# Kernel optimization log

Hardware: AMD Instinct MI355X
Metric: run time of the kernel (lower is better)

The kernel has to match this reference:

```python
import jax, jax.numpy as jnp
import numpy as np

EPS = 1e-6

def oneplus(x):
    return 1.0 + jnp.log1p(jnp.exp(x) + EPS)

def content_addr(mem, keys, strength):
    # mem [B,N,M], keys [B,R,M], strength [B,R] -> [B,R,N]
    mn = jnp.sqrt(jnp.sum(mem * mem, -1))    # [B,N]
    kn = jnp.sqrt(jnp.sum(keys * keys, -1))  # [B,R]
    sim = jnp.einsum('brm,bnm->brn', keys, mem) / (kn[..., None] * mn[:, None, :] + EPS)
    return jax.nn.softmax(strength[..., None] * sim, axis=-1)

def setup_inputs() -> dict:
    key = jax.random.key(0)
    ks = jax.random.split(key, 16)
    B, T, W, R, N, M = 16, 32, 128, 4, 512, 128
    def lin(k, fi, fo):
        k1, k2 = jax.random.split(k)
        s = 1.0 / np.sqrt(fi)
        return (jax.random.uniform(k1, (fi, fo), minval=-s, maxval=s),
                jax.random.uniform(k2, (fo,), minval=-s, maxval=s))
    Din = W + R * W  # controller input: cat(x_t, prev_reads)
    Wb, bb = lin(ks[0], Din + W, W)     # CfC backbone (1 layer, silu)
    Wff1, bff1 = lin(ks[1], W, W)
    Wff2, bff2 = lin(ks[2], W, W)
    Wta, bta = lin(ks[3], W, W)
    Wtb, btb = lin(ks[4], W, W)
    Wv, bv = lin(ks[5], W, W)
    Wr, br = lin(ks[6], W * R, W)
    Wxi, bxi = lin(ks[7], W, W * R + 3 * W + 5 * R + 3)
    X = jax.random.normal(ks[8], (B, T, W), dtype=jnp.float32)
    hs = jnp.zeros((B, W), dtype=jnp.float32)
    mem = jax.random.normal(ks[9], (B, N, M), dtype=jnp.float32) * 0.1
    reset_idxs = jax.random.randint(ks[10], (B, T), 0, 2, dtype=jnp.int32)
    return {'X': X, 'hs': hs, 'mem': mem, 'reset_idxs': reset_idxs,
            'Wb': Wb, 'bb': bb, 'Wff1': Wff1, 'bff1': bff1, 'Wff2': Wff2, 'bff2': bff2,
            'Wta': Wta, 'bta': bta, 'Wtb': Wtb, 'btb': btb,
            'Wv': Wv, 'bv': bv, 'Wr': Wr, 'br': br, 'Wxi': Wxi, 'bxi': bxi}

def dnc_forward(X, hs, mem, reset_idxs, Wb, bb, Wff1, bff1, Wff2, bff2,
                Wta, bta, Wtb, btb, Wv, bv, Wr, br, Wxi, bxi):
    B, T, W = X.shape
    N, M = mem.shape[1], mem.shape[2]
    R = (bxi.shape[0] - 3 * W - 3) // (W + 5)
    eye = jnp.eye(N, dtype=mem.dtype)

    def step(carry, inp):
        hs, memv, prev_reads, prev_rw, prev_ww, usage, prec, link = carry
        x_t, reset, t = inp
        r = reset.astype(x_t.dtype)
        memv = memv * (1 - r)[:, None, None]   # memory.reset_idx
        hs = hs * (1 - r)[:, None]
        # CfC controller cell
        z = jax.nn.silu(jnp.concatenate([x_t, prev_reads, hs], -1) @ Wb + bb)
        ff1 = z @ Wff1 + bff1
        ff2 = z @ Wff2 + bff2
        ti = jax.nn.sigmoid((z @ Wta + bta) * t + (z @ Wtb + btb))
        hs = ff1 * (1 - ti) + ti * ff2
        # interface vector split
        xi = hs @ Wxi + bxi
        p = 0
        read_keys = xi[:, :W * R].reshape(B, R, W); p = W * R
        write_key = xi[:, p:p + W]; p += W
        write_vec = xi[:, p:p + W]; p += W
        erase = jax.nn.sigmoid(xi[:, p:p + W]); p += W
        free_g = jax.nn.sigmoid(xi[:, p:p + R]); p += R
        read_str = oneplus(xi[:, p:p + R]); p += R
        read_modes = jax.nn.softmax(xi[:, p:p + 3 * R].reshape(B, R, 3), -1); p += 3 * R
        write_str = oneplus(xi[:, p:p + 1]); p += 1
        alloc_g = jax.nn.sigmoid(xi[:, p:p + 1]); p += 1
        write_g = jax.nn.sigmoid(xi[:, p:p + 1])
        # write weights
        wca = content_addr(memv, write_key[:, None, :], write_str)[:, 0]  # [B,N]
        retention = jnp.prod(1 - free_g[:, :, None] * prev_rw, axis=1)
        usage = (usage + prev_ww - usage * prev_ww) * retention
        si = jnp.argsort(usage, -1)
        cp = jnp.cumprod(jnp.take_along_axis(usage, si, -1), -1)
        alloc = (1 - usage) * jnp.take_along_axis(cp, si, -1)  # gather(1, sorted_idx), as in source
        ww = write_g * (alloc_g * alloc + (1 - alloc_g) * wca)  # [B,N]
        wc = ww[:, :, None]
        link = (1 - wc - jnp.swapaxes(wc, 1, 2)) * link + wc * prec[:, None, :]
        link = link * (1 - eye)
        prec = (1 - ww.sum(-1, keepdims=True)) * prec + ww
        memv = memv * (1 - wc * erase[:, None, :]) + wc * write_vec[:, None, :]
        # read
        rca = content_addr(memv, read_keys, read_str)              # [B,R,N]
        fw = jnp.einsum('brn,bnk->brk', prev_rw, link)
        bw = jnp.einsum('brn,bkn->brk', prev_rw, link)
        aux = jnp.stack([bw, rca, fw], 2)                          # [B,R,3,N]
        rw = (aux * read_modes[..., None]).sum(2)
        reads = jnp.einsum('brn,bnm->brm', rw, memv).reshape(B, R * M)
        y = hs @ Wv + bv + reads @ Wr + br
        # prev_reads is detached each step in the source
        carry = (hs, memv, jax.lax.stop_gradient(reads), rw, ww, usage, prec, link)
        return carry, (y, hs)

    dt = X.dtype
    init = (hs, mem,
            jnp.zeros((B, R * W), dt), jnp.zeros((B, R, N), dt), jnp.zeros((B, N), dt),
            jnp.zeros((B, N), dt), jnp.zeros((B, N), dt), jnp.zeros((B, N, N), dt))
    xs = (jnp.swapaxes(X, 0, 1), jnp.swapaxes(reset_idxs, 0, 1), jnp.arange(T, dtype=dt))
    _, (ys, hss) = jax.lax.scan(step, init, xs)
    return jnp.swapaxes(ys, 0, 1), jnp.swapaxes(hss, 0, 1)

def reference(X, hs, mem, reset_idxs, Wb, bb, Wff1, bff1, Wff2, bff2,
              Wta, bta, Wtb, btb, Wv, bv, Wr, br, Wxi, bxi):
    return dnc_forward(X, hs, mem, reset_idxs, Wb, bb, Wff1, bff1, Wff2, bff2,
                       Wta, bta, Wtb, btb, Wv, bv, Wr, br, Wxi, bxi)
```

## Files before the change

kernel.cpp:

```cpp
#include <hip/hip_runtime.h>
#include <math.h>

#define Bq 16
#define Tq 32
#define Wq 128
#define Rq 4
#define Nq 512
#define Mq 128
#define DINq 768
#define XIDq 919
#define BTWq (Bq*Tq*Wq)

#define TSTRIDE 31232
#define TF_FW    0
#define TF_BW    16384
#define TF_RCA   18432
#define TF_RW    20480
#define TF_PR    22528
#define TF_WC    26624
#define TF_WW    27136
#define TF_PREC  27648
#define TF_XI    28672
#define TF_CNT   29696

struct P {
  const float *X, *hs0, *mem0;
  const int *rst;
  const float *Wb,*bb,*Wff1,*bff1,*Wff2,*bff2,*Wta,*bta,*Wtb,*btb,*Wv,*bv,*Wr,*br,*Wxi,*bxi;
  float *out;
  float *rdh,*teams;
  float *WbT,*Wff1T,*Wff2T,*WtaT,*WtbT,*WvT,*WrT,*WxiT;
};

__device__ __forceinline__ float dot4(float4 a, float4 b){
  return a.x*b.x + a.y*b.y + a.z*b.z + a.w*b.w;
}
__device__ __forceinline__ float sigf(float x){ return 1.f/(1.f+expf(-x)); }
__device__ __forceinline__ float oneplusf(float x){ return 1.f + log1pf(expf(x) + 1e-6f); }

__device__ __forceinline__ void pst(float* p, float v){
  __hip_atomic_store(p, v, __ATOMIC_RELAXED, __HIP_MEMORY_SCOPE_AGENT);
}
__device__ __forceinline__ float pld(float* p){
  return __hip_atomic_load(p, __ATOMIC_RELAXED, __HIP_MEMORY_SCOPE_AGENT);
}
__device__ __forceinline__ void bump(unsigned* f){
  __syncthreads();
  if (threadIdx.x==0)
    __hip_atomic_fetch_add(f, 1u, __ATOMIC_RELAXED, __HIP_MEMORY_SCOPE_AGENT);
}
__device__ __forceinline__ void waitge(unsigned* f, unsigned v){
  if (threadIdx.x==0){
    while (__hip_atomic_load(f, __ATOMIC_RELAXED, __HIP_MEMORY_SCOPE_AGENT) < v)
      __builtin_amdgcn_s_sleep(1);
  }
  __syncthreads();
}

__device__ __forceinline__ float wave_sum64(float v){
  #pragma unroll
  for (int m=32;m>=1;m>>=1) v += __shfl_xor(v, m, 64);
  return v;
}
__device__ __forceinline__ float wave_max64(float v){
  #pragma unroll
  for (int m=32;m>=1;m>>=1) v = fmaxf(v, __shfl_xor(v, m, 64));
  return v;
}
__device__ __forceinline__ float blk_sum(float v, float* s8){
  int w = threadIdx.x>>6;
  v = wave_sum64(v);
  if ((threadIdx.x&63)==0) s8[w] = v;
  __syncthreads();
  float r = s8[0]+s8[1]+s8[2]+s8[3]+s8[4]+s8[5]+s8[6]+s8[7];
  __syncthreads();
  return r;
}
__device__ __forceinline__ float blk_max(float v, float* s8){
  int w = threadIdx.x>>6;
  v = wave_max64(v);
  if ((threadIdx.x&63)==0) s8[w] = v;
  __syncthreads();
  float r = s8[0];
  #pragma unroll
  for (int q=1;q<8;q++) r = fmaxf(r, s8[q]);
  __syncthreads();
  return r;
}
__device__ __forceinline__ float red_cg(float v){
  v += __shfl_xor(v, 1, 8);
  v += __shfl_xor(v, 2, 8);
  v += __shfl_xor(v, 4, 8);
  return v;
}

__global__ __launch_bounds__(256) void k_init(P p){
  int bid=blockIdx.x, tid=threadIdx.x;
  if (bid<8){ int idx=bid*256+tid, st=8*256;
    for (int k=idx;k<DINq*Wq;k+=st){ int j=k/DINq,i=k%DINq; p.WbT[k]=p.Wb[i*Wq+j]; }
  } else if (bid<10){ int idx=(bid-8)*256+tid, st=2*256;
    for (int k=idx;k<Wq*Wq;k+=st){ int j=k/Wq,i=k%Wq; p.Wff1T[k]=p.Wff1[i*Wq+j]; }
  } else if (bid<12){ int idx=(bid-10)*256+tid, st=2*256;
    for (int k=idx;k<Wq*Wq;k+=st){ int j=k/Wq,i=k%Wq; p.Wff2T[k]=p.Wff2[i*Wq+j]; }
  } else if (bid<14){ int idx=(bid-12)*256+tid, st=2*256;
    for (int k=idx;k<Wq*Wq;k+=st){ int j=k/Wq,i=k%Wq; p.WtaT[k]=p.Wta[i*Wq+j]; }
  } else if (bid<16){ int idx=(bid-14)*256+tid, st=2*256;
    for (int k=idx;k<Wq*Wq;k+=st){ int j=k/Wq,i=k%Wq; p.WtbT[k]=p.Wtb[i*Wq+j]; }
  } else if (bid<18){ int idx=(bid-16)*256+tid, st=2*256;
    for (int k=idx;k<Wq*Wq;k+=st){ int j=k/Wq,i=k%Wq; p.WvT[k]=p.Wv[i*Wq+j]; }
  } else if (bid<22){ int idx=(bid-18)*256+tid, st=4*256;
    for (int k=idx;k<Rq*Wq*Wq;k+=st){ int j=k/(Rq*Wq),i=k%(Rq*Wq); p.WrT[k]=p.Wr[i*Wq+j]; }
  } else if (bid<30){ int idx=(bid-22)*256+tid, st=8*256;
    for (int k=idx;k<XIDq*Wq;k+=st){ int f=k/Wq,i=k%Wq; p.WxiT[k]=p.Wxi[i*XIDq+f]; }
  } else if (bid<38){ int idx=(bid-30)*256+tid, st=8*256;
    for (int k=idx;k<16*TSTRIDE;k+=st) p.teams[k]=0.f;
  }
}

__global__ __launch_bounds__(512,2) void k_run(P p){
  const int tid=threadIdx.x, bid=blockIdx.x;
  const bool isA = (bid<16);
  const int team = isA ? bid : ((bid-16)>>3);
  const int g    = isA ? 0   : ((bid-16)&7);
  const int b=team;
  const int w=tid>>6, l=tid&63;
  float* T = p.teams + (size_t)team*TSTRIDE;
  unsigned* C = (unsigned*)(T+TF_CNT);
  unsigned* CNT_FW=C+0; unsigned* FLAG_RW=C+32; unsigned* CNT_RD=C+64;
  unsigned* FLAG_XI=C+96; unsigned* CNT_WC=C+128; unsigned* FLAG_WW=C+160;

  __shared__ __align__(16) float rwl[Rq*Nq];
  __shared__ __align__(16) float xil[XIDq+9];
  __shared__ __align__(16) float wwl[Nq];
  __shared__ __align__(16) float precl[Nq];
  __shared__ __align__(16) float usage[Nq];
  __shared__ __align__(16) float uarr[Nq];
  __shared__ __align__(16) float cpl[Nq];
  __shared__ __align__(16) int   sidx[Nq];
  __shared__ __align__(16) float wcas[Nq];
  __shared__ __align__(16) float inv[DINq];
  __shared__ __align__(16) float zl[Wq];
  __shared__ __align__(16) float hsl[Wq];
  __shared__ __align__(16) float acc4[4*Wq];
  __shared__ __align__(16) float scrA[Rq*Nq];
  __shared__ __align__(16) float scrB[Rq*Nq];
  __shared__ __align__(16) float scrC[Rq*Nq];
  __shared__ float s8[8];

  if (isA){
    for (int i=tid;i<Rq*Nq;i+=512) rwl[i]=0.f;
    usage[tid]=0.f; precl[tid]=0.f; wwl[tid]=0.f;
    if (tid<Wq) hsl[tid]=p.hs0[b*Wq+tid];
    __syncthreads();

    for (int t=0;t<=Tq;t++){
      if (t>0){
        waitge(CNT_FW, 8u*(unsigned)t);
        float* rcl=scrA; float* fwl=scrB; float* bwl=scrC;
        #pragma unroll
        for (int k=0;k<4;k++){
          int idx=tid+k*512;
          float f=0.f;
          #pragma unroll
          for (int gg=0;gg<8;gg++) f+=pld(T+TF_FW+gg*2048+idx);
          fwl[idx]=f;
          bwl[idx]=pld(T+TF_BW+idx);
          rcl[idx]=pld(T+TF_RCA+idx);
        }
        __syncthreads();
        #pragma unroll
        for (int r=0;r<Rq;r++){
          float v=rcl[r*Nq+tid];
          float mx=blk_max(v,s8);
          float e=expf(v-mx);
          float se=blk_sum(e,s8);
          rcl[r*Nq+tid]=e/se;
        }
        __syncthreads();
        #pragma unroll
        for (int k=0;k<4;k++){
          int idx=tid+k*512, r=idx>>9;
          float m0=xil[904+r*3],m1=xil[905+r*3],m2=xil[906+r*3];
          float mm=fmaxf(m0,fmaxf(m1,m2));
          float e0=expf(m0-mm),e1=expf(m1-mm),e2=expf(m2-mm);
          float es=e0+e1+e2;
          float rwv=(e0*bwl[idx]+e1*rcl[idx]+e2*fwl[idx])/es;
          rwl[idx]=rwv;
          pst(T+TF_RW+idx,rwv);
        }
      } else {
        #pragma unroll
        for (int k=0;k<4;k++){ int idx=tid+k*512; rwl[idx]=0.f; pst(T+TF_RW+idx,0.f); }
      }
      bump(FLAG_RW);
      if (t<Tq){
        float keep=1.f-(float)p.rst[b*Tq+t];
        if (tid<Wq){ inv[tid]=p.X[((size_t)b*Tq+t)*Wq+tid]; inv[Wq+Nq+tid]=keep*hsl[tid]; }
        __syncthreads();
        int j=tid>>2,q=tid&3;
        const float4* w4=(const float4*)(p.WbT+(size_t)j*DINq);
        const float4* i4=(const float4*)inv;
        float a=0.f;
        #pragma unroll
        for (int c=q;c<32;c+=4) a+=dot4(w4[c],i4[c]);
        #pragma unroll
        for (int c=160+q;c<192;c+=4) a+=dot4(w4[c],i4[c]);
        a+=__shfl_xor(a,1,4); a+=__shfl_xor(a,2,4);
        if (q==0) zl[j]=a+p.bb[j];
      }
      waitge(CNT_RD, 8u*(unsigned)(t+1));
      if (t>0){
        float s=0.f;
        #pragma unroll
        for (int gg=0;gg<8;gg++) s+=pld(T+TF_PR+gg*512+tid);
        inv[Wq+tid]=s;
        p.rdh[((size_t)b*Tq+(t-1))*Nq+tid]=s;
      } else inv[Wq+tid]=0.f;
      if (t==Tq) break;
      __syncthreads();
      { int j=tid>>2,q=tid&3;
        const float4* w4=(const float4*)(p.WbT+(size_t)j*DINq);
        const float4* i4=(const float4*)inv;
        float a=0.f;
        for (int c=32+q;c<160;c+=4) a+=dot4(w4[c],i4[c]);
        a+=__shfl_xor(a,1,4); a+=__shfl_xor(a,2,4);
        if (q==0){ float z=zl[j]+a; zl[j]=z*sigf(z); }
      }
      __syncthreads();
      { int which=tid>>7,j=tid&127;
        const float* Wg=(which==0)?p.Wff1T:(which==1)?p.Wff2T:(which==2)?p.WtaT:p.WtbT;
        const float4* w4=(const float4*)(Wg+(size_t)j*Wq);
        const float4* z4=(const float4*)zl;
        float a=0.f;
        #pragma unroll 8
        for (int c=0;c<32;c++) a+=dot4(w4[c],z4[c]);
        acc4[which*Wq+j]=a;
      }
      __syncthreads();
      if (tid<Wq){
        float a1=acc4[tid]+p.bff1[tid],a2=acc4[Wq+tid]+p.bff2[tid];
        float aa=acc4[2*Wq+tid]+p.bta[tid],ab=acc4[3*Wq+tid]+p.btb[tid];
        float ti=sigf(aa*(float)t+ab);
        float h=a1*(1.f-ti)+ti*a2;
        hsl[tid]=h;
        p.out[BTWq+((size_t)b*Tq+t)*Wq+tid]=h;
      }
      __syncthreads();
      { const float4* h4=(const float4*)hsl;
        { int o=tid>>2, q=tid&3; int f=512+o;
          const float4* w4=(const float4*)(p.WxiT+(size_t)f*Wq);
          float a=0.f;
          #pragma unroll
          for (int c=q;c<32;c+=4) a+=dot4(w4[c],h4[c]);
          a+=__shfl_xor(a,1,4); a+=__shfl_xor(a,2,4);
          if (q==0){ a+=p.bxi[f]; xil[f]=a; pst(T+TF_XI+f,a); }
        }
        if (tid<92){ int o=tid>>2, q=tid&3; int f=896+o;
          const float4* w4=(const float4*)(p.WxiT+(size_t)f*Wq);
          float a=0.f;
          #pragma unroll
          for (int c=q;c<32;c+=4) a+=dot4(w4[c],h4[c]);
          a+=__shfl_xor(a,1,4); a+=__shfl_xor(a,2,4);
          if (q==0){ a+=p.bxi[f]; xil[f]=a; pst(T+TF_XI+f,a); }
        }
      }
      bump(FLAG_XI);
      { const float4* h4=(const float4*)hsl;
        { const float4* w4=(const float4*)(p.WxiT+(size_t)tid*Wq);
          float a=p.bxi[tid];
          #pragma unroll 8
          for (int c=0;c<32;c++) a+=dot4(w4[c],h4[c]);
          xil[tid]=a; pst(T+TF_XI+tid,a);
        }
        if (tid<256){ int f=640+tid;
          const float4* w4=(const float4*)(p.WxiT+(size_t)f*Wq);
          float a=p.bxi[f];
          #pragma unroll 8
          for (int c=0;c<32;c++) a+=dot4(w4[c],h4[c]);
          xil[f]=a; pst(T+TF_XI+f,a);
        }
      }
      __syncthreads();
      int n=tid;
      float ret=1.f;
      #pragma unroll
      for (int r=0;r<Rq;r++) ret*=1.f-sigf(xil[896+r])*rwl[r*Nq+n];
      float uo=usage[n],pw=wwl[n];
      float u=(uo+pw-uo*pw)*ret;
      usage[n]=u; uarr[n]=u;
      __syncthreads();
      int rank=0;
      const float4* u4=(const float4*)uarr;
      #pragma unroll 8
      for (int jj=0;jj<128;jj++){
        float4 vv=u4[jj]; int j0=jj*4;
        rank+=(vv.x<u)||(vv.x==u&&(j0+0)<n);
        rank+=(vv.y<u)||(vv.y==u&&(j0+1)<n);
        rank+=(vv.z<u)||(vv.z==u&&(j0+2)<n);
        rank+=(vv.w<u)||(vv.w==u&&(j0+3)<n);
      }
      sidx[rank]=n;
      __syncthreads();
      int si=sidx[n];
      float sv=uarr[si];
      float x=sv;
      #pragma unroll
      for (int dd=1;dd<64;dd<<=1){ float pr=__shfl_up(x,dd,64); if (l>=dd) x*=pr; }
      if (l==63) s8[w]=x;
      __syncthreads();
      float woff=1.f;
      #pragma unroll
      for (int q=0;q<8;q++) if (q<w) woff*=s8[q];
      x*=woff;
      cpl[n]=x;
      waitge(CNT_WC, 8u*(unsigned)(t+1));
      { float v=pld(T+TF_WC+tid);
        float mx=blk_max(v,s8);
        float e=expf(v-mx);
        float se=blk_sum(e,s8);
        wcas[tid]=e/se;
      }
      __syncthreads();
      float alloc=(1.f-u)*cpl[si];
      float ag=sigf(xil[917]),wg=sigf(xil[918]);
      float wwv=wg*(ag*alloc+(1.f-ag)*wcas[n]);
      wwl[n]=wwv;
      pst(T+TF_WW+n,wwv);
      float wsum=blk_sum(wwv,s8);
      float pn=(1.f-wsum)*precl[n]+wwv;
      precl[n]=pn;
      pst(T+TF_PREC+(t&1)*Nq+n,pn);
      bump(FLAG_WW);
    }
  } else {
    const int rg=l>>3, cg=l&7;
    const int n_own=g*64+w*8+rg;
    const int c0=cg*16;
    float4 m4[4]; float nrm;
    { const float4* src=(const float4*)(p.mem0+((size_t)b*Nq+n_own)*Mq+c0);
      float s=0.f;
      #pragma unroll
      for (int i=0;i<4;i++){ m4[i]=src[i]; s+=dot4(m4[i],m4[i]); }
      nrm=sqrtf(red_cg(s));
    }
    float Lreg[8][8];
    #pragma unroll
    for (int rr=0;rr<8;rr++)
      #pragma unroll
      for (int q=0;q<8;q++) Lreg[rr][q]=0.f;

    for (int t=0;t<=Tq;t++){
      waitge(FLAG_RW, (unsigned)(t+1));
      for (int i=tid;i<Rq*Nq;i+=512) rwl[i]=pld(T+TF_RW+i);
      float* prl=wcas;
      prl[tid]=0.f;
      __syncthreads();
      #pragma unroll
      for (int r=0;r<Rq;r++){
        float rwn=rwl[r*Nq+n_own];
        #pragma unroll
        for (int i=0;i<4;i++){
          float ax=rwn*m4[i].x, ay=rwn*m4[i].y, az=rwn*m4[i].z, aw=rwn*m4[i].w;
          ax+=__shfl_xor(ax,8,64); ax+=__shfl_xor(ax,16,64); ax+=__shfl_xor(ax,32,64);
          ay+=__shfl_xor(ay,8,64); ay+=__shfl_xor(ay,16,64); ay+=__shfl_xor(ay,32,64);
          az+=__shfl_xor(az,8,64); az+=__shfl_xor(az,16,64); az+=__shfl_xor(az,32,64);
          aw+=__shfl_xor(aw,8,64); aw+=__shfl_xor(aw,16,64); aw+=__shfl_xor(aw,32,64);
          if (rg==0){
            atomicAdd(&prl[r*Wq+c0+i*4+0],ax);
            atomicAdd(&prl[r*Wq+c0+i*4+1],ay);
            atomicAdd(&prl[r*Wq+c0+i*4+2],az);
            atomicAdd(&prl[r*Wq+c0+i*4+3],aw);
          }
        }
      }
      __syncthreads();
      pst(T+TF_PR+g*512+tid, prl[tid]);
      bump(CNT_RD);
      if (t==Tq) break;
      waitge(FLAG_XI, (unsigned)(t+1));
      if (tid<Wq) xil[512+tid]=pld(T+TF_XI+512+tid);
      if (tid<23) xil[896+tid]=pld(T+TF_XI+896+tid);
      __syncthreads();
      float keep=1.f-(float)p.rst[b*Tq+t];
      { float kk=(tid<Wq)? xil[512+tid]*xil[512+tid]:0.f;
        float kn=sqrtf(blk_sum(kk,s8));
        const float4* k4=(const float4*)(xil+512);
        float d=0.f;
        #pragma unroll
        for (int i=0;i<4;i++) d+=dot4(k4[cg*4+i],m4[i]);
        d=red_cg(d);
        float wstr=oneplusf(xil[916]);
        float sim=(keep*d)/(kn*(keep*nrm)+1e-6f);
        if (cg==0) pst(T+TF_WC+n_own, wstr*sim);
      }
      bump(CNT_WC);
      precl[tid]=pld(T+TF_PREC+((t&1)^1)*Nq+tid);
      waitge(FLAG_WW,(unsigned)(t+1));
      wwl[tid]=pld(T+TF_WW+tid);
      xil[tid]=pld(T+TF_XI+tid);
      if (tid<256) xil[640+tid]=pld(T+TF_XI+640+tid);
      __syncthreads();
      { float* fwacc=scrA;
        int c0p=l*8;
        float ww8[8],pc8[8],pr8[Rq][8];
        *(float4*)&ww8[0]=*(const float4*)&wwl[c0p];   *(float4*)&ww8[4]=*(const float4*)&wwl[c0p+4];
        *(float4*)&pc8[0]=*(const float4*)&precl[c0p]; *(float4*)&pc8[4]=*(const float4*)&precl[c0p+4];
        #pragma unroll
        for (int r=0;r<Rq;r++){
          *(float4*)&pr8[r][0]=*(const float4*)&rwl[r*Nq+c0p];
          *(float4*)&pr8[r][4]=*(const float4*)&rwl[r*Nq+c0p+4];
        }
        float fa[Rq][8];
        #pragma unroll
        for (int r=0;r<Rq;r++)
          #pragma unroll
          for (int q=0;q<8;q++) fa[r][q]=0.f;
        #pragma unroll
        for (int rr=0;rr<8;rr++){
          int n2=g*64+w*8+rr;
          float wwn=wwl[n2];
          float prn[Rq];
          #pragma unroll
          for (int r=0;r<Rq;r++) prn[r]=rwl[r*Nq+n2];
          float bwp[Rq]={0.f,0.f,0.f,0.f};
          #pragma unroll
          for (int q=0;q<8;q++){
            float nv=(1.f-wwn-ww8[q])*Lreg[rr][q]+wwn*pc8[q];
            if (c0p+q==n2) nv=0.f;
            Lreg[rr][q]=nv;
            #pragma unroll
            for (int r=0;r<Rq;r++){ fa[r][q]+=prn[r]*nv; bwp[r]+=pr8[r][q]*nv; }
          }
          #pragma unroll
          for (int mm=1;mm<64;mm<<=1)
            #pragma unroll
            for (int r=0;r<Rq;r++) bwp[r]+=__shfl_xor(bwp[r],mm,64);
          if (l==0){
            #pragma unroll
            for (int r=0;r<Rq;r++) pst(T+TF_BW+r*Nq+n2, bwp[r]);
          }
        }
        for (int k=0;k<8;k++){
          if (w==k){
            #pragma unroll
            for (int r=0;r<Rq;r++)
              #pragma unroll
              for (int q=0;q<8;q++){
                if (k==0) fwacc[r*Nq+c0p+q]=fa[r][q];
                else      fwacc[r*Nq+c0p+q]+=fa[r][q];
              }
          }
          __syncthreads();
        }
        for (int i=tid;i<Rq*Nq;i+=512) pst(T+TF_FW+g*2048+i,fwacc[i]);
      }
      { float wwn=wwl[n_own];
        float s=0.f;
        #pragma unroll
        for (int i=0;i<4;i++){
          float e0=sigf(xil[768+c0+i*4+0]), e1=sigf(xil[768+c0+i*4+1]);
          float e2=sigf(xil[768+c0+i*4+2]), e3=sigf(xil[768+c0+i*4+3]);
          m4[i].x=m4[i].x*keep*(1.f-wwn*e0)+wwn*xil[640+c0+i*4+0];
          m4[i].y=m4[i].y*keep*(1.f-wwn*e1)+wwn*xil[640+c0+i*4+1];
          m4[i].z=m4[i].z*keep*(1.f-wwn*e2)+wwn*xil[640+c0+i*4+2];
          m4[i].w=m4[i].w*keep*(1.f-wwn*e3)+wwn*xil[640+c0+i*4+3];
          s+=dot4(m4[i],m4[i]);
        }
        nrm=sqrtf(red_cg(s));
        float kn4[Rq], rstr[Rq];
        #pragma unroll
        for (int r=0;r<Rq;r++){
          float kk=(tid<Wq)? xil[r*Wq+tid]*xil[r*Wq+tid]:0.f;
          kn4[r]=sqrtf(blk_sum(kk,s8));
          rstr[r]=oneplusf(xil[900+r]);
        }
        #pragma unroll
        for (int r=0;r<Rq;r++){
          const float4* kr=(const float4*)(xil+r*Wq);
          float d=0.f;
          #pragma unroll
          for (int i=0;i<4;i++) d+=dot4(kr[cg*4+i],m4[i]);
          d=red_cg(d);
          float v=rstr[r]*(d/(kn4[r]*nrm+1e-6f));
          if (cg==0) pst(T+TF_RCA+r*Nq+n_own, v);
        }
      }
      bump(CNT_FW);
    }
  }
}

__global__ __launch_bounds__(512) void k_y(P p){
  int j=blockIdx.x, tid=threadIdx.x;
  __shared__ __align__(16) float wv[Wq];
  __shared__ __align__(16) float wr[Rq*Wq];
  if (tid<Wq) wv[tid]=p.WvT[(size_t)j*Wq+tid];
  wr[tid]=p.WrT[(size_t)j*(Rq*Wq)+tid];
  __syncthreads();
  int b=tid>>5, t=tid&31;
  const float4* h4=(const float4*)(p.out+BTWq+((size_t)b*Tq+t)*Wq);
  const float4* r4=(const float4*)(p.rdh+((size_t)b*Tq+t)*Nq);
  const float4* wv4=(const float4*)wv;
  const float4* wr4=(const float4*)wr;
  float a=0.f;
  #pragma unroll 8
  for (int c=0;c<32;c++) a+=dot4(wv4[c],h4[c]);
  #pragma unroll 8
  for (int c=0;c<128;c++) a+=dot4(wr4[c],r4[c]);
  p.out[((size_t)b*Tq+t)*Wq+j]=a+p.bv[j]+p.br[j];
}

extern "C" void kernel_launch(void* const* d_in, const int* in_sizes, int n_in,
                              void* d_out, int out_size, void* d_ws, size_t ws_size,
                              hipStream_t stream){
  (void)in_sizes; (void)n_in; (void)out_size; (void)ws_size;
  P p;
  p.X    = (const float*)d_in[0];
  p.hs0  = (const float*)d_in[1];
  p.mem0 = (const float*)d_in[2];
  p.rst  = (const int*)d_in[3];
  p.Wb   = (const float*)d_in[4];  p.bb   = (const float*)d_in[5];
  p.Wff1 = (const float*)d_in[6];  p.bff1 = (const float*)d_in[7];
  p.Wff2 = (const float*)d_in[8];  p.bff2 = (const float*)d_in[9];
  p.Wta  = (const float*)d_in[10]; p.bta  = (const float*)d_in[11];
  p.Wtb  = (const float*)d_in[12]; p.btb  = (const float*)d_in[13];
  p.Wv   = (const float*)d_in[14]; p.bv   = (const float*)d_in[15];
  p.Wr   = (const float*)d_in[16]; p.br   = (const float*)d_in[17];
  p.Wxi  = (const float*)d_in[18]; p.bxi  = (const float*)d_in[19];
  p.out  = (float*)d_out;
  float* ws = (float*)d_ws;
  size_t o = 0;
  p.rdh   = ws + o; o += (size_t)Bq*Tq*Nq;
  p.teams = ws + o; o += (size_t)16*TSTRIDE;
  p.WbT   = ws + o; o += (size_t)DINq*Wq;
  p.Wff1T = ws + o; o += (size_t)Wq*Wq;
  p.Wff2T = ws + o; o += (size_t)Wq*Wq;
  p.WtaT  = ws + o; o += (size_t)Wq*Wq;
  p.WtbT  = ws + o; o += (size_t)Wq*Wq;
  p.WvT   = ws + o; o += (size_t)Wq*Wq;
  p.WrT   = ws + o; o += (size_t)Rq*Wq*Wq;
  p.WxiT  = ws + o; o += (size_t)XIDq*Wq;

  hipLaunchKernelGGL(k_init, dim3(38),  dim3(256), 0, stream, p);
  hipLaunchKernelGGL(k_run,  dim3(144), dim3(512), 0, stream, p);
  hipLaunchKernelGGL(k_y,    dim3(128), dim3(512), 0, stream, p);
}
```

Before: 2.476 ms.

## Move read-vector backbone matvec to worker blocks and split link/rca waits

Worker blocks now compute their partial contribution of the previous reads to the controller backbone preactivation (WbT times partial reads) and publish it, so the controller block only sums eight 128-length partials instead of doing a 512-wide matvec on the critical path. The write of read history to global memory is deferred to after the write-weight phase. A new counter lets the controller load forward and backward link results before the read content scores are ready. Together these aim to shorten the serial controller path, at the cost of extra scratch space, another counter and more work per worker.

```diff
diff --git a/kernel.cpp b/kernel.cpp
--- a/kernel.cpp
+++ b/kernel.cpp
@@ -21,7 +21,8 @@
 #define TF_WW    27136
 #define TF_PREC  27648
 #define TF_XI    28672
-#define TF_CNT   29696
+#define TF_ZP    29696
+#define TF_CNT   30720
 
 struct P {
   const float *X, *hs0, *mem0;
@@ -128,6 +129,7 @@
   unsigned* C = (unsigned*)(T+TF_CNT);
   unsigned* CNT_FW=C+0; unsigned* FLAG_RW=C+32; unsigned* CNT_RD=C+64;
   unsigned* FLAG_XI=C+96; unsigned* CNT_WC=C+128; unsigned* FLAG_WW=C+160;
+  unsigned* CNT_LNK=C+192;
 
   __shared__ __align__(16) float rwl[Rq*Nq];
   __shared__ __align__(16) float xil[XIDq+9];
@@ -155,8 +157,8 @@
 
     for (int t=0;t<=Tq;t++){
       if (t>0){
-        waitge(CNT_FW, 8u*(unsigned)t);
         float* rcl=scrA; float* fwl=scrB; float* bwl=scrC;
+        waitge(CNT_LNK, 8u*(unsigned)t);
         #pragma unroll
         for (int k=0;k<4;k++){
           int idx=tid+k*512;
@@ -165,6 +167,11 @@
           for (int gg=0;gg<8;gg++) f+=pld(T+TF_FW+gg*2048+idx);
           fwl[idx]=f;
           bwl[idx]=pld(T+TF_BW+idx);
+        }
+        waitge(CNT_FW, 8u*(unsigned)t);
+        #pragma unroll
+        for (int k=0;k<4;k++){
+          int idx=tid+k*512;
           rcl[idx]=pld(T+TF_RCA+idx);
         }
         __syncthreads();
@@ -209,22 +216,19 @@
         if (q==0) zl[j]=a+p.bb[j];
       }
       waitge(CNT_RD, 8u*(unsigned)(t+1));
-      if (t>0){
+      if (t==Tq){
         float s=0.f;
         #pragma unroll
         for (int gg=0;gg<8;gg++) s+=pld(T+TF_PR+gg*512+tid);
-        inv[Wq+tid]=s;
-        p.rdh[((size_t)b*Tq+(t-1))*Nq+tid]=s;
-      } else inv[Wq+tid]=0.f;
-      if (t==Tq) break;
-      __syncthreads();
-      { int j=tid>>2,q=tid&3;
-        const float4* w4=(const float4*)(p.WbT+(size_t)j*DINq);
-        const float4* i4=(const float4*)inv;
-        float a=0.f;
-        for (int c=32+q;c<160;c+=4) a+=dot4(w4[c],i4[c]);
-        a+=__shfl_xor(a,1,4); a+=__shfl_xor(a,2,4);
-        if (q==0){ float z=zl[j]+a; zl[j]=z*sigf(z); }
+        p.rdh[((size_t)b*Tq+(Tq-1))*Nq+tid]=s;
+        break;
+      }
+      if (tid<Wq){
+        float zr=0.f;
+        #pragma unroll
+        for (int gg=0;gg<8;gg++) zr+=pld(T+TF_ZP+gg*128+tid);
+        float z=zl[tid]+zr;
+        zl[tid]=z*sigf(z);
       }
       __syncthreads();
       { int which=tid>>7,j=tid&127;
@@ -331,6 +335,12 @@
       precl[n]=pn;
       pst(T+TF_PREC+(t&1)*Nq+n,pn);
       bump(FLAG_WW);
+      if (t>0){
+        float s=0.f;
+        #pragma unroll
+        for (int gg=0;gg<8;gg++) s+=pld(T+TF_PR+gg*512+tid);
+        p.rdh[((size_t)b*Tq+(t-1))*Nq+tid]=s;
+      }
     }
   } else {
     const int rg=l>>3, cg=l&7;
@@ -375,6 +385,15 @@
       }
       __syncthreads();
       pst(T+TF_PR+g*512+tid, prl[tid]);
+      { int j=tid>>2, q=tid&3;
+        const float4* w4=(const float4*)(p.WbT+(size_t)j*DINq);
+        const float4* pr4=(const float4*)prl;
+        float a=0.f;
+        #pragma unroll
+        for (int c=0;c<32;c++) a+=dot4(w4[32+q*32+c], pr4[q*32+c]);
+        a+=__shfl_xor(a,1,4); a+=__shfl_xor(a,2,4);
+        if (q==0) pst(T+TF_ZP+g*128+j, a);
+      }
       bump(CNT_RD);
       if (t==Tq) break;
       waitge(FLAG_XI, (unsigned)(t+1));
@@ -454,6 +473,7 @@
         }
         for (int i=tid;i<Rq*Nq;i+=512) pst(T+TF_FW+g*2048+i,fwacc[i]);
       }
+      bump(CNT_LNK);
       { float wwn=wwl[n_own];
         float s=0.f;
         #pragma unroll
```

Result: slower. 2.533 ms (+2.3%).
